# Optimization experiments

Measured on AMD Instinct MI355X. Metric: run time of the kernel, lower is better.

Reference implementation:

```python
import jax, jax.numpy as jnp
import numpy as np

N_NODES = 50000
N_EDGES = 800000
N_FEAT = 128
N_HIDDEN = 128
N_CLASSES = 64


def sage_mean_conv(x, src, dst, W_self, W_neigh, b, n_nodes):
    # DGL SAGEConv (mean): out = x @ W_self + mean_neigh(x) @ W_neigh + b
    # mean over in-neighbors: messages flow src -> dst
    msg = x[src]  # [E, F] gather
    h_sum = jax.ops.segment_sum(msg, dst, num_segments=n_nodes)  # [N, F]
    deg = jax.ops.segment_sum(jnp.ones((src.shape[0],), x.dtype), dst,
                              num_segments=n_nodes)
    h_mean = h_sum / jnp.maximum(deg, 1.0)[:, None]
    return x @ W_self + h_mean @ W_neigh + b


def setup_inputs() -> dict:
    key = jax.random.key(0)
    ks = jax.random.split(key, 8)
    sc1 = 1.0 / np.sqrt(N_FEAT)
    sc2 = 1.0 / np.sqrt(N_HIDDEN)
    return {
        "x": jax.random.normal(ks[0], (N_NODES, N_FEAT), jnp.float32),
        "W_self1": jax.random.normal(ks[1], (N_FEAT, N_HIDDEN), jnp.float32) * sc1,
        "W_neigh1": jax.random.normal(ks[2], (N_FEAT, N_HIDDEN), jnp.float32) * sc1,
        "b1": jnp.zeros((N_HIDDEN,), jnp.float32),
        "W_self2": jax.random.normal(ks[3], (N_HIDDEN, N_CLASSES), jnp.float32) * sc2,
        "W_neigh2": jax.random.normal(ks[4], (N_HIDDEN, N_CLASSES), jnp.float32) * sc2,
        "b2": jnp.zeros((N_CLASSES,), jnp.float32),
        "src": jax.random.randint(ks[5], (N_EDGES,), 0, N_NODES, jnp.int32),
        "dst": jax.random.randint(ks[6], (N_EDGES,), 0, N_NODES, jnp.int32),
    }


def reference(x, W_self1, W_neigh1, b1, W_self2, W_neigh2, b2, src, dst):
    n = x.shape[0]
    h = sage_mean_conv(x, src, dst, W_self1, W_neigh1, b1, n)
    h = jax.nn.relu(h)
    logits = sage_mean_conv(h, src, dst, W_self2, W_neigh2, b2, n)
    return logits
```

## Files before the change

### kernel.cpp

```cpp
#include <hip/hip_runtime.h>
#include <hip/hip_fp16.h>

#define N_NODES 50000
#define N_EDGES 800000
#define N_FEAT 128
#define N_HIDDEN 128
#define N_CLASSES 64

#define NBUCK 256
#define BUCK_NODES 196
#define BIN_CHUNK 2048
#define BIN_BLK ((N_EDGES + BIN_CHUNK - 1) / BIN_CHUNK)

#define CAST_BLK 6250
#define PACK1_BLK 16
#define PACK2_BLK 8
#define PREP_BLK (CAST_BLK + BIN_BLK + PACK1_BLK + PACK2_BLK)
#define GEMM1_BLK ((N_NODES + 31) / 32)
#define BG_BLK (BIN_BLK + GEMM1_BLK)

typedef __attribute__((ext_vector_type(8))) short bf16x8;
typedef __attribute__((ext_vector_type(4))) float f32x4;
typedef __attribute__((ext_vector_type(2))) float f32x2;

__device__ __forceinline__ unsigned short f32_to_bf16(float f) {
    unsigned int u = __float_as_uint(f);
    return (unsigned short)((u + 0x7fffu + ((u >> 16) & 1u)) >> 16);
}
__device__ __forceinline__ float bf16lo(unsigned int v) { return __uint_as_float(v << 16); }
__device__ __forceinline__ float bf16hi(unsigned int v) { return __uint_as_float(v & 0xffff0000u); }

#if defined(__has_builtin)
#if __has_builtin(__builtin_amdgcn_cvt_pk_f32_fp8) && __has_builtin(__builtin_amdgcn_cvt_pk_fp8_f32)
#define FP8_HW 1
#endif
#endif

__device__ __forceinline__ unsigned char f32_to_fp8(float f) {
#ifdef FP8_HW
    return (unsigned char)(__builtin_amdgcn_cvt_pk_fp8_f32(f, f, 0, false) & 0xff);
#else
    unsigned short hb = __half_as_ushort(__float2half(f));
    return (unsigned char)((hb + 0x7fu + ((hb >> 8) & 1u)) >> 8);
#endif
}

__device__ __forceinline__ void fp8x4_to_f32(unsigned int u, float* o) {
#ifdef FP8_HW
    f32x2 lo = __builtin_amdgcn_cvt_pk_f32_fp8(u, false);
    f32x2 hi = __builtin_amdgcn_cvt_pk_f32_fp8(u, true);
    o[0] = lo.x; o[1] = lo.y; o[2] = hi.x; o[3] = hi.y;
#else
    o[0] = __half2float(__ushort_as_half((unsigned short)((u & 0xffu) << 8)));
    o[1] = __half2float(__ushort_as_half((unsigned short)(((u >> 8) & 0xffu) << 8)));
    o[2] = __half2float(__ushort_as_half((unsigned short)(((u >> 16) & 0xffu) << 8)));
    o[3] = __half2float(__ushort_as_half((unsigned short)(((u >> 24) & 0xffu) << 8)));
#endif
}

template <int NOUT>
__device__ void pack_w_body(int idx, const float* __restrict__ Wself,
                            const float* __restrict__ Wneigh,
                            unsigned short* __restrict__ Bp) {
    constexpr int NT = NOUT / 16;
    constexpr int NO = NOUT / 2;
    if (idx >= 4 * NT * 64) return;
    const int lane = idx & 63;
    const int tc = idx >> 6;
    const int c = tc % NT;
    const int t = tc / NT;
    const int n = c * 16 + (lane & 15);
    const int k0 = t * 32 + (lane >> 4) * 8;
    const float* W = (n < NO) ? Wself : Wneigh;
    const int nn = (n < NO) ? n : n - NO;
    ushort4 lo, hi;
    lo.x = f32_to_bf16(W[(k0 + 0) * NO + nn]);
    lo.y = f32_to_bf16(W[(k0 + 1) * NO + nn]);
    lo.z = f32_to_bf16(W[(k0 + 2) * NO + nn]);
    lo.w = f32_to_bf16(W[(k0 + 3) * NO + nn]);
    hi.x = f32_to_bf16(W[(k0 + 4) * NO + nn]);
    hi.y = f32_to_bf16(W[(k0 + 5) * NO + nn]);
    hi.z = f32_to_bf16(W[(k0 + 6) * NO + nn]);
    hi.w = f32_to_bf16(W[(k0 + 7) * NO + nn]);
    ((ushort4*)&Bp[(size_t)idx * 8])[0] = lo;
    ((ushort4*)&Bp[(size_t)idx * 8])[1] = hi;
}

__device__ void a0_body(int blk, const int* __restrict__ dst, int* __restrict__ hists) {
    __shared__ int h[NBUCK];
    const int t = threadIdx.x;
    h[t] = 0;
    __syncthreads();
    const int lo = blk * BIN_CHUNK;
    const int hi = min(lo + BIN_CHUNK, N_EDGES);
    for (int i = lo + t; i < hi; i += 256) {
        atomicAdd(&h[dst[i] / BUCK_NODES], 1);
    }
    __syncthreads();
    hists[blk * NBUCK + t] = h[t];
}

__global__ __launch_bounds__(256) void prep_kernel(
        const float* __restrict__ x, unsigned short* __restrict__ xb,
        const int* __restrict__ dst, int* __restrict__ hists,
        const float* __restrict__ Ws1, const float* __restrict__ Wn1,
        unsigned short* __restrict__ Bp1,
        const float* __restrict__ Ws2, const float* __restrict__ Wn2,
        unsigned short* __restrict__ Bp2) {
    const int b = blockIdx.x;
    const int t = threadIdx.x;
    if (b < CAST_BLK) {
        int i = b * 256 + t;
        float4 v = ((const float4*)x)[i];
        ushort4 o;
        o.x = f32_to_bf16(v.x);
        o.y = f32_to_bf16(v.y);
        o.z = f32_to_bf16(v.z);
        o.w = f32_to_bf16(v.w);
        ((ushort4*)xb)[i] = o;
    } else if (b < CAST_BLK + BIN_BLK) {
        a0_body(b - CAST_BLK, dst, hists);
    } else if (b < CAST_BLK + BIN_BLK + PACK1_BLK) {
        int idx = (b - CAST_BLK - BIN_BLK) * 256 + t;
        pack_w_body<256>(idx, Ws1, Wn1, Bp1);
    } else {
        int idx = (b - CAST_BLK - BIN_BLK - PACK1_BLK) * 256 + t;
        pack_w_body<128>(idx, Ws2, Wn2, Bp2);
    }
}

__global__ __launch_bounds__(256) void bscan_kernel(const int* __restrict__ hists,
                                                    int* __restrict__ bstart,
                                                    int* __restrict__ bcursor) {
    __shared__ int sc[NBUCK];
    const int t = threadIdx.x;
    int v = 0;
#pragma unroll 8
    for (int c = 0; c < BIN_BLK; ++c) v += hists[c * NBUCK + t];
    sc[t] = v;
    __syncthreads();
    for (int s = 1; s < NBUCK; s <<= 1) {
        int u = (t >= s) ? sc[t - s] : 0;
        __syncthreads();
        sc[t] += u;
        __syncthreads();
    }
    const int excl = sc[t] - v;
    bstart[t] = excl;
    bcursor[t] = excl;
    if (t == NBUCK - 1) bstart[NBUCK] = sc[t];
}

__device__ void a1_body(int blk, const int* __restrict__ src, const int* __restrict__ dst,
                        const int* __restrict__ hists,
                        int* __restrict__ bcursor, unsigned int* __restrict__ binned) {
    __shared__ int base[NBUCK];
    __shared__ int cnt[NBUCK];
    const int t = threadIdx.x;
    const int h = hists[blk * NBUCK + t];
    base[t] = atomicAdd(&bcursor[t], h);
    cnt[t] = 0;
    __syncthreads();
    const int lo = blk * BIN_CHUNK;
    const int hi = min(lo + BIN_CHUNK, N_EDGES);
    for (int i = lo + t; i < hi; i += 256) {
        const int d = dst[i];
        const int b = d / BUCK_NODES;
        const int r = atomicAdd(&cnt[b], 1);
        binned[base[b] + r] = ((unsigned int)(d - b * BUCK_NODES) << 16) | (unsigned int)src[i];
    }
}

template <int NOUT, bool PFP8>
__device__ void gemm_mfma_body(int gblk,
                               const unsigned short* __restrict__ xb,
                               const unsigned short* __restrict__ Bp,
                               const float* __restrict__ bias,
                               float* __restrict__ s,
                               unsigned char* __restrict__ p8,
                               unsigned short* __restrict__ p16) {
    constexpr int NT = NOUT / 16;
    constexpr int NO = NOUT / 2;
    constexpr int NSUB = NT / 4;

    const int tid = threadIdx.x;
    const int wave = tid >> 6;
    const int lane = tid & 63;
    const int mcol = lane & 15;
    const int kgrp = lane >> 4;

    const int mbase = gblk * 32;
    int r0 = mbase + mcol;       if (r0 >= N_NODES) r0 = N_NODES - 1;
    int r1 = mbase + 16 + mcol;  if (r1 >= N_NODES) r1 = N_NODES - 1;

    f32x4 acc[2][NSUB];
#pragma unroll
    for (int mt = 0; mt < 2; ++mt)
#pragma unroll
        for (int c = 0; c < NSUB; ++c)
            acc[mt][c] = (f32x4){0.f, 0.f, 0.f, 0.f};

#pragma unroll
    for (int t = 0; t < 4; ++t) {
        bf16x8 a0 = *(const bf16x8*)&xb[(size_t)r0 * 128 + t * 32 + kgrp * 8];
        bf16x8 a1 = *(const bf16x8*)&xb[(size_t)r1 * 128 + t * 32 + kgrp * 8];
#pragma unroll
        for (int c = 0; c < NSUB; ++c) {
            const int ct = wave * NSUB + c;
            bf16x8 bfrag = *(const bf16x8*)&Bp[((size_t)(t * NT + ct) * 64 + lane) * 8];
            acc[0][c] = __builtin_amdgcn_mfma_f32_16x16x32_bf16(a0, bfrag, acc[0][c], 0, 0, 0);
            acc[1][c] = __builtin_amdgcn_mfma_f32_16x16x32_bf16(a1, bfrag, acc[1][c], 0, 0, 0);
        }
    }

    float bv[NSUB];
    int ncols[NSUB];
#pragma unroll
    for (int c = 0; c < NSUB; ++c) {
        ncols[c] = (wave * NSUB + c) * 16 + mcol;
        bv[c] = (ncols[c] < NO) ? bias[ncols[c]] : 0.f;
    }

#pragma unroll
    for (int mt = 0; mt < 2; ++mt) {
#pragma unroll
        for (int c = 0; c < NSUB; ++c) {
            const int ncol = ncols[c];
#pragma unroll
            for (int r = 0; r < 4; ++r) {
                const int node = mbase + mt * 16 + kgrp * 4 + r;
                if (node >= N_NODES) continue;
                const float v = acc[mt][c][r];
                if (ncol < NO) {
                    s[(size_t)node * NO + ncol] = v + bv[c];
                } else if (PFP8) {
                    p8[(size_t)node * NO + (ncol - NO)] = f32_to_fp8(v);
                } else {
                    p16[(size_t)node * NO + (ncol - NO)] = f32_to_bf16(v);
                }
            }
        }
    }
}

__global__ __launch_bounds__(256) void bin_gemm1_kernel(
        const int* __restrict__ src, const int* __restrict__ dst,
        const int* __restrict__ hists,
        int* __restrict__ bcursor, unsigned int* __restrict__ binned,
        const unsigned short* __restrict__ xb,
        const unsigned short* __restrict__ Bp1,
        const float* __restrict__ b1,
        float* __restrict__ s1, unsigned char* __restrict__ p1) {
    const int b = blockIdx.x;
    if (b < BIN_BLK) {
        a1_body(b, src, dst, hists, bcursor, binned);
    } else {
        gemm_mfma_body<256, true>(b - BIN_BLK, xb, Bp1, b1, s1, p1, nullptr);
    }
}

__global__ __launch_bounds__(256) void bucket_build_kernel(
        const unsigned int* __restrict__ binned,
        const int* __restrict__ bstart,
        int* __restrict__ offsets,
        unsigned short* __restrict__ csr16) {
    __shared__ int cnt[NBUCK];
    __shared__ int pre[NBUCK];
    const int b = blockIdx.x;
    const int t = threadIdx.x;
    const int n0 = b * BUCK_NODES;
    const int nn = min(N_NODES - n0, BUCK_NODES);
    const int e0 = bstart[b];
    const int e1 = bstart[b + 1];

    cnt[t] = 0;
    __syncthreads();
    for (int i = e0 + t; i < e1; i += 256) {
        atomicAdd(&cnt[binned[i] >> 16], 1);
    }
    __syncthreads();
    int v = cnt[t];
    pre[t] = v;
    __syncthreads();
    for (int s = 1; s < NBUCK; s <<= 1) {
        int u = (t >= s) ? pre[t - s] : 0;
        __syncthreads();
        pre[t] += u;
        __syncthreads();
    }
    const int excl = pre[t] - v;
    if (t < nn) offsets[n0 + t] = e0 + excl;
    if (b == 0 && t == 0) offsets[N_NODES] = N_EDGES;
    __syncthreads();
    pre[t] = excl;
    cnt[t] = 0;
    __syncthreads();
    for (int i = e0 + t; i < e1; i += 256) {
        const unsigned int u = binned[i];
        const int dl = (int)(u >> 16);
        const int r = atomicAdd(&cnt[dl], 1);
        csr16[e0 + pre[dl] + r] = (unsigned short)(u & 0xffffu);
    }
}

__global__ __launch_bounds__(256) void gemm2_kernel(
        const unsigned short* __restrict__ h1b,
        const unsigned short* __restrict__ Bp2,
        const float* __restrict__ b2,
        float* __restrict__ s2, unsigned short* __restrict__ p2) {
    gemm_mfma_body<128, false>(blockIdx.x, h1b, Bp2, b2, s2, nullptr, p2);
}

__global__ __launch_bounds__(256) void agg_relu_128_kernel(
        const float* __restrict__ s,
        const unsigned char* __restrict__ p,
        const int* __restrict__ offsets,
        const unsigned short* __restrict__ csr16,
        unsigned short* __restrict__ h1b) {
    const int wave = threadIdx.x >> 6;
    const int lane = threadIdx.x & 63;
    const int q = lane >> 4;
    const int l = lane & 15;
    const int node = blockIdx.x * 4 + wave;
    if (node >= N_NODES) return;

    const int off0 = offsets[node];
    const int off1 = offsets[node + 1];
    const uint2* pp = (const uint2*)p;

    float a[8];
#pragma unroll
    for (int k = 0; k < 8; ++k) a[k] = 0.f;

    for (int i = off0 + q; i < off1; i += 32) {
        int idx[8];
        float m[8];
        uint2 w[8];
#pragma unroll
        for (int j = 0; j < 8; ++j) {
            const int e = i + 4 * j;
            const int ec = min(e, off1 - 1);
            idx[j] = (int)csr16[ec];
            m[j] = (e < off1) ? 1.f : 0.f;
        }
#pragma unroll
        for (int j = 0; j < 8; ++j) w[j] = pp[(size_t)idx[j] * 16 + l];
#pragma unroll
        for (int j = 0; j < 8; ++j) {
            float d0[4], d1[4];
            fp8x4_to_f32(w[j].x, d0);
            fp8x4_to_f32(w[j].y, d1);
            a[0] += m[j] * d0[0]; a[1] += m[j] * d0[1];
            a[2] += m[j] * d0[2]; a[3] += m[j] * d0[3];
            a[4] += m[j] * d1[0]; a[5] += m[j] * d1[1];
            a[6] += m[j] * d1[2]; a[7] += m[j] * d1[3];
        }
    }
#pragma unroll
    for (int k = 0; k < 8; ++k) {
        a[k] += __shfl_xor(a[k], 16);
        a[k] += __shfl_xor(a[k], 32);
    }

    if (q == 0) {
        const float invdeg = 1.0f / fmaxf((float)(off1 - off0), 1.0f);
        float4 s0 = ((const float4*)s)[(size_t)node * 32 + l * 2];
        float4 s1 = ((const float4*)s)[(size_t)node * 32 + l * 2 + 1];
        ushort4 o0, o1;
        o0.x = f32_to_bf16(fmaxf(s0.x + a[0] * invdeg, 0.f));
        o0.y = f32_to_bf16(fmaxf(s0.y + a[1] * invdeg, 0.f));
        o0.z = f32_to_bf16(fmaxf(s0.z + a[2] * invdeg, 0.f));
        o0.w = f32_to_bf16(fmaxf(s0.w + a[3] * invdeg, 0.f));
        o1.x = f32_to_bf16(fmaxf(s1.x + a[4] * invdeg, 0.f));
        o1.y = f32_to_bf16(fmaxf(s1.y + a[5] * invdeg, 0.f));
        o1.z = f32_to_bf16(fmaxf(s1.z + a[6] * invdeg, 0.f));
        o1.w = f32_to_bf16(fmaxf(s1.w + a[7] * invdeg, 0.f));
        ((ushort4*)h1b)[(size_t)node * 32 + l * 2] = o0;
        ((ushort4*)h1b)[(size_t)node * 32 + l * 2 + 1] = o1;
    }
}

__global__ __launch_bounds__(256) void agg_64_kernel(
        const unsigned short* __restrict__ p,
        const int* __restrict__ offsets,
        const unsigned short* __restrict__ csr16,
        float* __restrict__ out) {
    const int wave = threadIdx.x >> 6;
    const int lane = threadIdx.x & 63;
    const int st = lane >> 3;
    const int l = lane & 7;
    const int node = blockIdx.x * 4 + wave;
    if (node >= N_NODES) return;

    const int off0 = offsets[node];
    const int off1 = offsets[node + 1];
    const uint4* pp = (const uint4*)p;

    float a[8];
#pragma unroll
    for (int k = 0; k < 8; ++k) a[k] = 0.f;

    for (int i = off0 + st; i < off1; i += 32) {
        int idx[4];
        float m[4];
        uint4 w[4];
#pragma unroll
        for (int j = 0; j < 4; ++j) {
            const int e = i + 8 * j;
            const int ec = min(e, off1 - 1);
            idx[j] = (int)csr16[ec];
            m[j] = (e < off1) ? 1.f : 0.f;
        }
#pragma unroll
        for (int j = 0; j < 4; ++j) w[j] = pp[(size_t)idx[j] * 8 + l];
#pragma unroll
        for (int j = 0; j < 4; ++j) {
            a[0] += m[j] * bf16lo(w[j].x); a[1] += m[j] * bf16hi(w[j].x);
            a[2] += m[j] * bf16lo(w[j].y); a[3] += m[j] * bf16hi(w[j].y);
            a[4] += m[j] * bf16lo(w[j].z); a[5] += m[j] * bf16hi(w[j].z);
            a[6] += m[j] * bf16lo(w[j].w); a[7] += m[j] * bf16hi(w[j].w);
        }
    }
#pragma unroll
    for (int k = 0; k < 8; ++k) {
        a[k] += __shfl_xor(a[k], 8);
        a[k] += __shfl_xor(a[k], 16);
        a[k] += __shfl_xor(a[k], 32);
    }

    if (st == 0) {
        const float invdeg = 1.0f / fmaxf((float)(off1 - off0), 1.0f);
        float4 s0 = ((float4*)out)[(size_t)node * 16 + l * 2];
        float4 s1 = ((float4*)out)[(size_t)node * 16 + l * 2 + 1];
        s0.x += a[0] * invdeg; s0.y += a[1] * invdeg;
        s0.z += a[2] * invdeg; s0.w += a[3] * invdeg;
        s1.x += a[4] * invdeg; s1.y += a[5] * invdeg;
        s1.z += a[6] * invdeg; s1.w += a[7] * invdeg;
        ((float4*)out)[(size_t)node * 16 + l * 2] = s0;
        ((float4*)out)[(size_t)node * 16 + l * 2 + 1] = s1;
    }
}

extern "C" void kernel_launch(void* const* d_in, const int* in_sizes, int n_in,
                              void* d_out, int out_size, void* d_ws, size_t ws_size,
                              hipStream_t stream) {
    const float* x        = (const float*)d_in[0];
    const float* W_self1  = (const float*)d_in[1];
    const float* W_neigh1 = (const float*)d_in[2];
    const float* b1       = (const float*)d_in[3];
    const float* W_self2  = (const float*)d_in[4];
    const float* W_neigh2 = (const float*)d_in[5];
    const float* b2       = (const float*)d_in[6];
    const int*   src      = (const int*)d_in[7];
    const int*   dst      = (const int*)d_in[8];
    float* out = (float*)d_out;

    int* bstart  = (int*)d_ws;
    int* bcursor = bstart + 288;
    int* offsets = bcursor + 256;
    int* hists   = offsets + 50048;
    unsigned int* binned = (unsigned int*)(hists + BIN_BLK * NBUCK);
    unsigned short* csr16 = (unsigned short*)(binned + 800000);
    unsigned short* Bp1 = csr16 + 800000;
    unsigned short* Bp2 = Bp1 + 32768;
    unsigned short* xb  = Bp2 + 16384;
    unsigned short* h1b = xb;
    float* s1 = (float*)(xb + (size_t)N_NODES * 128);
    unsigned char* p1 = (unsigned char*)(s1 + (size_t)N_NODES * 128);
    unsigned short* p2 = (unsigned short*)p1;

    prep_kernel<<<PREP_BLK, 256, 0, stream>>>(x, xb, dst, hists,
                                              W_self1, W_neigh1, Bp1,
                                              W_self2, W_neigh2, Bp2);
    bscan_kernel<<<1, 256, 0, stream>>>(hists, bstart, bcursor);
    bin_gemm1_kernel<<<BG_BLK, 256, 0, stream>>>(src, dst, hists, bcursor, binned,
                                                 xb, Bp1, b1, s1, p1);
    bucket_build_kernel<<<NBUCK, 256, 0, stream>>>(binned, bstart, offsets, csr16);
    agg_relu_128_kernel<<<(N_NODES + 3) / 4, 256, 0, stream>>>(s1, p1, offsets, csr16, h1b);
    gemm2_kernel<<<(N_NODES + 31) / 32, 256, 0, stream>>>(h1b, Bp2, b2, out, p2);
    agg_64_kernel<<<(N_NODES + 3) / 4, 256, 0, stream>>>(p2, offsets, csr16, out);
}
```

Measured before the change: 207.8 us.

## Fuse x bf16 cast into GEMM1 A-load and store self term as bf16

Removes the separate cast pass over x in the prep kernel; GEMM1 now reads fp32 x directly and converts to bf16 in registers before the MFMA. The self-term output s1 is stored as bf16 instead of fp32, halving its write and the later read in the first aggregation kernel. The cost is doubled A-operand read bytes inside GEMM1 (each row read once per wave), plus an extra bf16 rounding of the self term that slightly reduces precision. Workspace layout is rearranged so h1b no longer aliases the cast buffer.

After: 208.0 us. No clear change (+0.1%).

```diff
diff --git a/kernel.cpp b/kernel.cpp
--- a/kernel.cpp
+++ b/kernel.cpp
@@ -12,10 +12,9 @@
 #define BIN_CHUNK 2048
 #define BIN_BLK ((N_EDGES + BIN_CHUNK - 1) / BIN_CHUNK)
 
-#define CAST_BLK 6250
 #define PACK1_BLK 16
 #define PACK2_BLK 8
-#define PREP_BLK (CAST_BLK + BIN_BLK + PACK1_BLK + PACK2_BLK)
+#define PREP_BLK (BIN_BLK + PACK1_BLK + PACK2_BLK)
 #define GEMM1_BLK ((N_NODES + 31) / 32)
 #define BG_BLK (BIN_BLK + GEMM1_BLK)
 
@@ -101,7 +100,6 @@
 }
 
 __global__ __launch_bounds__(256) void prep_kernel(
-        const float* __restrict__ x, unsigned short* __restrict__ xb,
         const int* __restrict__ dst, int* __restrict__ hists,
         const float* __restrict__ Ws1, const float* __restrict__ Wn1,
         unsigned short* __restrict__ Bp1,
@@ -109,22 +107,13 @@
         unsigned short* __restrict__ Bp2) {
     const int b = blockIdx.x;
     const int t = threadIdx.x;
-    if (b < CAST_BLK) {
-        int i = b * 256 + t;
-        float4 v = ((const float4*)x)[i];
-        ushort4 o;
-        o.x = f32_to_bf16(v.x);
-        o.y = f32_to_bf16(v.y);
-        o.z = f32_to_bf16(v.z);
-        o.w = f32_to_bf16(v.w);
-        ((ushort4*)xb)[i] = o;
-    } else if (b < CAST_BLK + BIN_BLK) {
-        a0_body(b - CAST_BLK, dst, hists);
-    } else if (b < CAST_BLK + BIN_BLK + PACK1_BLK) {
-        int idx = (b - CAST_BLK - BIN_BLK) * 256 + t;
+    if (b < BIN_BLK) {
+        a0_body(b, dst, hists);
+    } else if (b < BIN_BLK + PACK1_BLK) {
+        int idx = (b - BIN_BLK) * 256 + t;
         pack_w_body<256>(idx, Ws1, Wn1, Bp1);
     } else {
-        int idx = (b - CAST_BLK - BIN_BLK - PACK1_BLK) * 256 + t;
+        int idx = (b - BIN_BLK - PACK1_BLK) * 256 + t;
         pack_w_body<128>(idx, Ws2, Wn2, Bp2);
     }
 }
@@ -171,12 +160,25 @@
     }
 }
 
-template <int NOUT, bool PFP8>
+__device__ __forceinline__ bf16x8 load_a_f32(const float* base) {
+    float4 u = ((const float4*)base)[0];
+    float4 v = ((const float4*)base)[1];
+    bf16x8 a;
+    a[0] = (short)f32_to_bf16(u.x); a[1] = (short)f32_to_bf16(u.y);
+    a[2] = (short)f32_to_bf16(u.z); a[3] = (short)f32_to_bf16(u.w);
+    a[4] = (short)f32_to_bf16(v.x); a[5] = (short)f32_to_bf16(v.y);
+    a[6] = (short)f32_to_bf16(v.z); a[7] = (short)f32_to_bf16(v.w);
+    return a;
+}
+
+template <int NOUT, bool AF32, bool SB16, bool PFP8>
 __device__ void gemm_mfma_body(int gblk,
-                               const unsigned short* __restrict__ xb,
+                               const float* __restrict__ af,
+                               const unsigned short* __restrict__ ab,
                                const unsigned short* __restrict__ Bp,
                                const float* __restrict__ bias,
-                               float* __restrict__ s,
+                               float* __restrict__ s32,
+                               unsigned short* __restrict__ s16,
                                unsigned char* __restrict__ p8,
                                unsigned short* __restrict__ p16) {
     constexpr int NT = NOUT / 16;
@@ -202,8 +204,14 @@
 
 #pragma unroll
     for (int t = 0; t < 4; ++t) {
-        bf16x8 a0 = *(const bf16x8*)&xb[(size_t)r0 * 128 + t * 32 + kgrp * 8];
-        bf16x8 a1 = *(const bf16x8*)&xb[(size_t)r1 * 128 + t * 32 + kgrp * 8];
+        bf16x8 a0, a1;
+        if (AF32) {
+            a0 = load_a_f32(&af[(size_t)r0 * 128 + t * 32 + kgrp * 8]);
+            a1 = load_a_f32(&af[(size_t)r1 * 128 + t * 32 + kgrp * 8]);
+        } else {
+            a0 = *(const bf16x8*)&ab[(size_t)r0 * 128 + t * 32 + kgrp * 8];
+            a1 = *(const bf16x8*)&ab[(size_t)r1 * 128 + t * 32 + kgrp * 8];
+        }
 #pragma unroll
         for (int c = 0; c < NSUB; ++c) {
             const int ct = wave * NSUB + c;
@@ -232,7 +240,8 @@
                 if (node >= N_NODES) continue;
                 const float v = acc[mt][c][r];
                 if (ncol < NO) {
-                    s[(size_t)node * NO + ncol] = v + bv[c];
+                    if (SB16) s16[(size_t)node * NO + ncol] = f32_to_bf16(v + bv[c]);
+                    else      s32[(size_t)node * NO + ncol] = v + bv[c];
                 } else if (PFP8) {
                     p8[(size_t)node * NO + (ncol - NO)] = f32_to_fp8(v);
                 } else {
@@ -247,15 +256,16 @@
         const int* __restrict__ src, const int* __restrict__ dst,
         const int* __restrict__ hists,
         int* __restrict__ bcursor, unsigned int* __restrict__ binned,
-        const unsigned short* __restrict__ xb,
+        const float* __restrict__ x,
         const unsigned short* __restrict__ Bp1,
         const float* __restrict__ b1,
-        float* __restrict__ s1, unsigned char* __restrict__ p1) {
+        unsigned short* __restrict__ s1, unsigned char* __restrict__ p1) {
     const int b = blockIdx.x;
     if (b < BIN_BLK) {
         a1_body(b, src, dst, hists, bcursor, binned);
     } else {
-        gemm_mfma_body<256, true>(b - BIN_BLK, xb, Bp1, b1, s1, p1, nullptr);
+        gemm_mfma_body<256, true, true, true>(b - BIN_BLK, x, nullptr, Bp1, b1,
+                                              nullptr, s1, p1, nullptr);
     }
 }
 
@@ -308,11 +318,12 @@
         const unsigned short* __restrict__ Bp2,
         const float* __restrict__ b2,
         float* __restrict__ s2, unsigned short* __restrict__ p2) {
-    gemm_mfma_body<128, false>(blockIdx.x, h1b, Bp2, b2, s2, nullptr, p2);
+    gemm_mfma_body<128, false, false, false>(blockIdx.x, nullptr, h1b, Bp2, b2,
+                                             s2, nullptr, nullptr, p2);
 }
 
 __global__ __launch_bounds__(256) void agg_relu_128_kernel(
-        const float* __restrict__ s,
+        const unsigned short* __restrict__ s16,
         const unsigned char* __restrict__ p,
         const int* __restrict__ offsets,
         const unsigned short* __restrict__ csr16,
@@ -364,17 +375,21 @@
 
     if (q == 0) {
         const float invdeg = 1.0f / fmaxf((float)(off1 - off0), 1.0f);
-        float4 s0 = ((const float4*)s)[(size_t)node * 32 + l * 2];
-        float4 s1 = ((const float4*)s)[(size_t)node * 32 + l * 2 + 1];
+        uint4 sw = ((const uint4*)s16)[(size_t)node * 16 + l];
+        float sf[8];
+        sf[0] = bf16lo(sw.x); sf[1] = bf16hi(sw.x);
+        sf[2] = bf16lo(sw.y); sf[3] = bf16hi(sw.y);
+        sf[4] = bf16lo(sw.z); sf[5] = bf16hi(sw.z);
+        sf[6] = bf16lo(sw.w); sf[7] = bf16hi(sw.w);
         ushort4 o0, o1;
-        o0.x = f32_to_bf16(fmaxf(s0.x + a[0] * invdeg, 0.f));
-        o0.y = f32_to_bf16(fmaxf(s0.y + a[1] * invdeg, 0.f));
-        o0.z = f32_to_bf16(fmaxf(s0.z + a[2] * invdeg, 0.f));
-        o0.w = f32_to_bf16(fmaxf(s0.w + a[3] * invdeg, 0.f));
-        o1.x = f32_to_bf16(fmaxf(s1.x + a[4] * invdeg, 0.f));
-        o1.y = f32_to_bf16(fmaxf(s1.y + a[5] * invdeg, 0.f));
-        o1.z = f32_to_bf16(fmaxf(s1.z + a[6] * invdeg, 0.f));
-        o1.w = f32_to_bf16(fmaxf(s1.w + a[7] * invdeg, 0.f));
+        o0.x = f32_to_bf16(fmaxf(sf[0] + a[0] * invdeg, 0.f));
+        o0.y = f32_to_bf16(fmaxf(sf[1] + a[1] * invdeg, 0.f));
+        o0.z = f32_to_bf16(fmaxf(sf[2] + a[2] * invdeg, 0.f));
+        o0.w = f32_to_bf16(fmaxf(sf[3] + a[3] * invdeg, 0.f));
+        o1.x = f32_to_bf16(fmaxf(sf[4] + a[4] * invdeg, 0.f));
+        o1.y = f32_to_bf16(fmaxf(sf[5] + a[5] * invdeg, 0.f));
+        o1.z = f32_to_bf16(fmaxf(sf[6] + a[6] * invdeg, 0.f));
+        o1.w = f32_to_bf16(fmaxf(sf[7] + a[7] * invdeg, 0.f));
         ((ushort4*)h1b)[(size_t)node * 32 + l * 2] = o0;
         ((ushort4*)h1b)[(size_t)node * 32 + l * 2 + 1] = o1;
     }
@@ -463,18 +478,17 @@
     unsigned short* csr16 = (unsigned short*)(binned + 800000);
     unsigned short* Bp1 = csr16 + 800000;
     unsigned short* Bp2 = Bp1 + 32768;
-    unsigned short* xb  = Bp2 + 16384;
-    unsigned short* h1b = xb;
-    float* s1 = (float*)(xb + (size_t)N_NODES * 128);
-    unsigned char* p1 = (unsigned char*)(s1 + (size_t)N_NODES * 128);
-    unsigned short* p2 = (unsigned short*)p1;
-
-    prep_kernel<<<PREP_BLK, 256, 0, stream>>>(x, xb, dst, hists,
+    unsigned short* s1  = Bp2 + 16384;
+    unsigned short* h1b = s1 + (size_t)N_NODES * 128;
+    unsigned char* p1   = (unsigned char*)(h1b + (size_t)N_NODES * 128);
+    unsigned short* p2  = (unsigned short*)p1;
+
+    prep_kernel<<<PREP_BLK, 256, 0, stream>>>(dst, hists,
                                               W_self1, W_neigh1, Bp1,
                                               W_self2, W_neigh2, Bp2);
     bscan_kernel<<<1, 256, 0, stream>>>(hists, bstart, bcursor);
     bin_gemm1_kernel<<<BG_BLK, 256, 0, stream>>>(src, dst, hists, bcursor, binned,
-                                                 xb, Bp1, b1, s1, p1);
+                                                 x, Bp1, b1, s1, p1);
     bucket_build_kernel<<<NBUCK, 256, 0, stream>>>(binned, bstart, offsets, csr16);
     agg_relu_128_kernel<<<(N_NODES + 3) / 4, 256, 0, stream>>>(s1, p1, offsets, csr16, h1b);
     gemm2_kernel<<<(N_NODES + 31) / 32, 256, 0, stream>>>(h1b, Bp2, b2, out, p2);
```
